# Kernel optimization log

Measured on AMD Instinct MI355X. Metric: run time of the kernel, lower is better.

## Reference

```python
import jax, jax.numpy as jnp
import numpy as np

B, S, D, H, W, FFN = 2, 4096, 1024, 16, 256, 4096
HD = D // H


def layer_norm(x, g, b):
    mu = x.mean(-1, keepdims=True)
    var = ((x - mu) ** 2).mean(-1, keepdims=True)
    return (x - mu) * jax.lax.rsqrt(var + 1e-5) * g + b


def setup_inputs() -> dict:
    key = jax.random.key(0)
    ks = jax.random.split(key, 16)
    s = 1.0 / np.sqrt(D)
    inp = {
        "x": jax.random.normal(ks[0], (B, S, D), jnp.float32),
        "Wq": jax.random.normal(ks[1], (D, D), jnp.float32) * s,
        "bq": jnp.zeros((D,), jnp.float32),
        "Wk": jax.random.normal(ks[2], (D, D), jnp.float32) * s,
        "bk": jnp.zeros((D,), jnp.float32),
        "Wv": jax.random.normal(ks[3], (D, D), jnp.float32) * s,
        "bv": jnp.zeros((D,), jnp.float32),
        "Wo": jax.random.normal(ks[4], (D, D), jnp.float32) * s,
        "bo": jnp.zeros((D,), jnp.float32),
        "g1": jnp.ones((D,), jnp.float32),
        "b1": jnp.zeros((D,), jnp.float32),
        "W1": jax.random.normal(ks[5], (D, FFN), jnp.float32) * s,
        "c1": jnp.zeros((FFN,), jnp.float32),
        "W2": jax.random.normal(ks[6], (FFN, D), jnp.float32) * (1.0 / np.sqrt(FFN)),
        "c2": jnp.zeros((D,), jnp.float32),
        "g2": jnp.ones((D,), jnp.float32),
        "b2": jnp.zeros((D,), jnp.float32),
    }
    return inp


def sliding_window_attn(x, Wq, bq, Wk, bk, Wv, bv, Wo, bo):
    b, s, d = x.shape
    nb = s // W
    # project and chunk into blocks of size W: (B, nb, W, H, HD)
    q = (x @ Wq + bq).reshape(b, nb, W, H, HD)
    k = (x @ Wk + bk).reshape(b, nb, W, H, HD)
    v = (x @ Wv + bv).reshape(b, nb, W, H, HD)
    pad = [(0, 0), (1, 1), (0, 0), (0, 0), (0, 0)]
    kp, vp = jnp.pad(k, pad), jnp.pad(v, pad)
    # each block attends to [prev, self, next] blocks -> (B, nb, 3W, H, HD)
    kc = jnp.concatenate([kp[:, :-2], kp[:, 1:-1], kp[:, 2:]], axis=2)
    vc = jnp.concatenate([vp[:, :-2], vp[:, 1:-1], vp[:, 2:]], axis=2)
    scale = jnp.asarray(1.0 / np.sqrt(HD), x.dtype)
    scores = jnp.einsum("bnqhd,bnkhd->bhnqk", q, kc) * scale
    i = jnp.arange(W)[:, None]
    j = jnp.arange(3 * W)[None, :]
    band = jnp.abs(i + W - j) <= W  # (W, 3W): |q_pos - k_pos| <= W
    kidx = jnp.arange(nb)[:, None] * W - W + jnp.arange(3 * W)[None, :]
    valid = (kidx >= 0) & (kidx < s)  # (nb, 3W): drop padded halo blocks
    mask = band[None, :, :] & valid[:, None, :]  # (nb, W, 3W)
    scores = jnp.where(mask[None, None], scores, jnp.asarray(-1e9, x.dtype))
    attn = jax.nn.softmax(scores, axis=-1)
    out = jnp.einsum("bhnqk,bnkhd->bnqhd", attn, vc).reshape(b, s, d)
    return out @ Wo + bo


def reference(x, Wq, bq, Wk, bk, Wv, bv, Wo, bo, g1, b1, W1, c1, W2, c2, g2, b2):
    a = sliding_window_attn(x, Wq, bq, Wk, bk, Wv, bv, Wo, bo)
    h = layer_norm(a + x, g1, b1)  # dropout = identity (eval mode)
    f = jax.nn.gelu(h @ W1 + c1) @ W2 + c2
    return layer_norm(f + h, g2, b2)
```

## Files before the change

### kernel.cpp

```cpp
#include <hip/hip_runtime.h>
#include <hip/hip_bf16.h>

#define BB 2
#define SS 4096
#define DD 1024
#define HH 16
#define WW 256
#define FF 4096
#define HDIM 64
#define NBLK (SS / WW)
#define MROWS (BB * SS)

typedef short bfrag8 __attribute__((ext_vector_type(8)));
typedef float floatx4 __attribute__((ext_vector_type(4)));

__device__ __forceinline__ float bf2f(ushort u) {
    union { uint i; float f; } c; c.i = ((uint)u) << 16; return c.f;
}
__device__ __forceinline__ ushort f2bf(float f) {
    union { float f; uint i; } c; c.f = f;
    uint r = (c.i + 0x7FFFu + ((c.i >> 16) & 1u)) >> 16;
    return (ushort)r;
}
__device__ __forceinline__ float gelu_tanh(float x) {
    float x3 = x * x * x;
    return 0.5f * x * (1.f + tanhf(0.7978845608028654f * (x + 0.044715f * x3)));
}

__device__ __forceinline__ void gload_lds16(const ushort* g, ushort* l) {
    __builtin_amdgcn_global_load_lds(
        (const __attribute__((address_space(1))) void*)g,
        (__attribute__((address_space(3))) void*)l, 16, 0, 0);
}

__global__ __launch_bounds__(256) void cvt_f32_bf16(
    const float* __restrict__ in, ushort* __restrict__ out)
{
    size_t i = ((size_t)blockIdx.x * 256 + threadIdx.x) * 4;
    float4 v = *(const float4*)(in + i);
    union { ushort u[4]; uint2 d; } t;
    t.u[0] = f2bf(v.x); t.u[1] = f2bf(v.y);
    t.u[2] = f2bf(v.z); t.u[3] = f2bf(v.w);
    *(uint2*)(out + i) = t.d;
}

__global__ __launch_bounds__(256) void cvt_transpose(
    const float* __restrict__ in, ushort* __restrict__ out, int K, int N)
{
    __shared__ ushort sT[32][33];
    const int n0 = blockIdx.x * 32, k0 = blockIdx.y * 32;
    const int r  = threadIdx.x >> 3;
    const int c4 = (threadIdx.x & 7) * 4;

    float4 v = *(const float4*)(in + (size_t)(k0 + r) * N + n0 + c4);
    sT[c4 + 0][r] = f2bf(v.x);
    sT[c4 + 1][r] = f2bf(v.y);
    sT[c4 + 2][r] = f2bf(v.z);
    sT[c4 + 3][r] = f2bf(v.w);
    __syncthreads();
    union { ushort u[4]; uint2 d; } t;
#pragma unroll
    for (int e = 0; e < 4; ++e) t.u[e] = sT[r][c4 + e];
    *(uint2*)(out + (size_t)(n0 + r) * K + k0 + c4) = t.d;
}

__global__ __launch_bounds__(256) void gemm_bt(
    const ushort* __restrict__ A, const ushort* __restrict__ Bt,
    const float* __restrict__ bias, ushort* __restrict__ C,
    int M, int N, int K, int act)
{
    __shared__ ushort sA[128 * 32];
    __shared__ ushort sB[128 * 32];

    const int tid  = threadIdx.x;
    const int m0   = blockIdx.y * 128;
    const int n0   = blockIdx.x * 128;
    const int wave = tid >> 6;
    const int lane = tid & 63;
    const int wm   = (wave >> 1) * 64;
    const int wn   = (wave & 1) * 64;
    const int lrow = lane & 15;
    const int quad = lane >> 4;

    floatx4 acc[4][4];
#pragma unroll
    for (int i = 0; i < 4; ++i)
#pragma unroll
        for (int j = 0; j < 4; ++j)
            acc[i][j] = (floatx4){0.f, 0.f, 0.f, 0.f};

    for (int k0 = 0; k0 < K; k0 += 32) {
#pragma unroll
        for (int it = 0; it < 2; ++it) {
            int c = it * 256 + tid;
            gload_lds16(A  + (size_t)(m0 + (c >> 2)) * K + k0 + (c & 3) * 8, &sA[c * 8]);
            gload_lds16(Bt + (size_t)(n0 + (c >> 2)) * K + k0 + (c & 3) * 8, &sB[c * 8]);
        }
        __syncthreads();

        bfrag8 af[4], bfv[4];
#pragma unroll
        for (int mt = 0; mt < 4; ++mt)
            af[mt] = *(const bfrag8*)&sA[(wm + mt * 16 + lrow) * 32 + quad * 8];
#pragma unroll
        for (int nt = 0; nt < 4; ++nt)
            bfv[nt] = *(const bfrag8*)&sB[(wn + nt * 16 + lrow) * 32 + quad * 8];
#pragma unroll
        for (int mt = 0; mt < 4; ++mt)
#pragma unroll
            for (int nt = 0; nt < 4; ++nt)
                acc[mt][nt] = __builtin_amdgcn_mfma_f32_16x16x32_bf16(
                    af[mt], bfv[nt], acc[mt][nt], 0, 0, 0);
        __syncthreads();
    }

#pragma unroll
    for (int nt = 0; nt < 4; ++nt) {
        int col = n0 + wn + nt * 16 + lrow;
        float bb = bias[col];
#pragma unroll
        for (int mt = 0; mt < 4; ++mt) {
#pragma unroll
            for (int r = 0; r < 4; ++r) {
                int row = m0 + wm + mt * 16 + (quad << 2) + r;
                float v = acc[mt][nt][r] + bb;
                if (act) v = gelu_tanh(v);
                C[(size_t)row * N + col] = f2bf(v);
            }
        }
    }
}

__global__ __launch_bounds__(256) void gemm_qkv(
    const ushort* __restrict__ A, const ushort* __restrict__ Bt,
    const float* __restrict__ bq, const float* __restrict__ bk,
    const float* __restrict__ bv,
    ushort* __restrict__ qb, ushort* __restrict__ kb, ushort* __restrict__ vT)
{
    __shared__ ushort sA[128 * 32];
    __shared__ ushort sB[128 * 32];
    const int K = DD, N = 3 * DD;

    const int tid  = threadIdx.x;
    const int m0   = blockIdx.y * 128;
    const int n0   = blockIdx.x * 128;
    const int wave = tid >> 6;
    const int lane = tid & 63;
    const int wm   = (wave >> 1) * 64;
    const int wn   = (wave & 1) * 64;
    const int lrow = lane & 15;
    const int quad = lane >> 4;

    floatx4 acc[4][4];
#pragma unroll
    for (int i = 0; i < 4; ++i)
#pragma unroll
        for (int j = 0; j < 4; ++j)
            acc[i][j] = (floatx4){0.f, 0.f, 0.f, 0.f};

    for (int k0 = 0; k0 < K; k0 += 32) {
#pragma unroll
        for (int it = 0; it < 2; ++it) {
            int c = it * 256 + tid;
            gload_lds16(A  + (size_t)(m0 + (c >> 2)) * K + k0 + (c & 3) * 8, &sA[c * 8]);
            gload_lds16(Bt + (size_t)(n0 + (c >> 2)) * K + k0 + (c & 3) * 8, &sB[c * 8]);
        }
        __syncthreads();

        bfrag8 af[4], bfv[4];
#pragma unroll
        for (int mt = 0; mt < 4; ++mt)
            af[mt] = *(const bfrag8*)&sA[(wm + mt * 16 + lrow) * 32 + quad * 8];
#pragma unroll
        for (int nt = 0; nt < 4; ++nt)
            bfv[nt] = *(const bfrag8*)&sB[(wn + nt * 16 + lrow) * 32 + quad * 8];
#pragma unroll
        for (int mt = 0; mt < 4; ++mt)
#pragma unroll
            for (int nt = 0; nt < 4; ++nt)
                acc[mt][nt] = __builtin_amdgcn_mfma_f32_16x16x32_bf16(
                    af[mt], bfv[nt], acc[mt][nt], 0, 0, 0);
        __syncthreads();
    }

    const int colbase = n0 + wn;
    const int sel = colbase >> 10;
    if (sel < 2) {
        ushort* C = (sel == 0) ? qb : kb;
        const float* bias = (sel == 0) ? bq : bk;
#pragma unroll
        for (int nt = 0; nt < 4; ++nt) {
            int cc = (colbase + nt * 16 + lrow) & 1023;
            float bb = bias[cc];
#pragma unroll
            for (int mt = 0; mt < 4; ++mt)
#pragma unroll
                for (int r = 0; r < 4; ++r) {
                    int row = m0 + wm + mt * 16 + (quad << 2) + r;
                    C[(size_t)row * DD + cc] = f2bf(acc[mt][nt][r] + bb);
                }
        }
    } else {
#pragma unroll
        for (int nt = 0; nt < 4; ++nt) {
            int cc = (colbase + nt * 16 + lrow) & 1023;
            int h = cc >> 6, dh = cc & 63;
            float bb = bv[cc];
#pragma unroll
            for (int mt = 0; mt < 4; ++mt) {
                int row0 = m0 + wm + mt * 16 + (quad << 2);
                int b = row0 >> 12, s = row0 & 4095;
                union { ushort u[4]; uint2 d; } t;
#pragma unroll
                for (int r = 0; r < 4; ++r) t.u[r] = f2bf(acc[mt][nt][r] + bb);
                *(uint2*)(vT + (size_t)(((b * HH + h) * HDIM + dh)) * SS + s) = t.d;
            }
        }
    }
}

__global__ __launch_bounds__(64, 2) void attn_flash(
    const ushort* __restrict__ q, const ushort* __restrict__ k,
    const ushort* __restrict__ vT, ushort* __restrict__ out)
{
    __shared__ ushort sP[64 * 72];

    const int qt = blockIdx.x, h = blockIdx.y, b = blockIdx.z;
    const int lane = threadIdx.x;
    const int c16  = lane & 15;
    const int quad = lane >> 4;
    const float CC = 0.18033688011112042f;

    bfrag8 qf[4][2];
    {
        const size_t qbase = ((size_t)b * SS + qt * 64) * DD + h * HDIM;
#pragma unroll
        for (int nt = 0; nt < 4; ++nt)
#pragma unroll
            for (int ks = 0; ks < 2; ++ks)
                qf[nt][ks] = *(const bfrag8*)(q + qbase +
                    (size_t)(nt * 16 + c16) * DD + ks * 32 + quad * 8);
    }

    floatx4 oacc[4][4];
#pragma unroll
    for (int i = 0; i < 4; ++i)
#pragma unroll
        for (int j = 0; j < 4; ++j)
            oacc[i][j] = (floatx4){0.f, 0.f, 0.f, 0.f};
    float mrow[4], lsum[4];
#pragma unroll
    for (int i = 0; i < 4; ++i) { mrow[i] = -1e30f; lsum[i] = 0.f; }

    const int st0 = (qt - 4 > 0) ? qt - 4 : 0;
    const int st1 = (qt + 4 < 63) ? qt + 4 : 63;
    const size_t kb_b  = (size_t)b * SS * DD + h * HDIM;
    const size_t vT_b  = (size_t)((b * HH + h) * HDIM) * SS;

    for (int st = st0; st <= st1; ++st) {
        const int dlt = st - qt;

        floatx4 sacc[4][4];
#pragma unroll
        for (int i = 0; i < 4; ++i)
#pragma unroll
            for (int j = 0; j < 4; ++j)
                sacc[i][j] = (floatx4){0.f, 0.f, 0.f, 0.f};
#pragma unroll
        for (int ks = 0; ks < 2; ++ks) {
            bfrag8 kf[4];
#pragma unroll
            for (int mt = 0; mt < 4; ++mt)
                kf[mt] = *(const bfrag8*)(k + kb_b +
                    (size_t)(st * 64 + mt * 16 + c16) * DD + ks * 32 + quad * 8);
#pragma unroll
            for (int mt = 0; mt < 4; ++mt)
#pragma unroll
                for (int nt = 0; nt < 4; ++nt)
                    sacc[mt][nt] = __builtin_amdgcn_mfma_f32_16x16x32_bf16(
                        kf[mt], qf[nt][ks], sacc[mt][nt], 0, 0, 0);
        }

        if (dlt == 4 || dlt == -4) {
#pragma unroll
            for (int mt = 0; mt < 4; ++mt)
#pragma unroll
                for (int nt = 0; nt < 4; ++nt)
#pragma unroll
                    for (int r = 0; r < 4; ++r) {
                        int kl = mt * 16 + quad * 4 + r;
                        int ql = nt * 16 + c16;
                        bool ok = (dlt < 0) ? (kl >= ql) : (kl <= ql);
                        if (!ok) sacc[mt][nt][r] = -1e30f;
                    }
        }

        float pm[4];
#pragma unroll
        for (int nt = 0; nt < 4; ++nt) {
            float a0 = fmaxf(fmaxf(sacc[0][nt][0], sacc[0][nt][1]),
                             fmaxf(sacc[0][nt][2], sacc[0][nt][3]));
            float a1 = fmaxf(fmaxf(sacc[1][nt][0], sacc[1][nt][1]),
                             fmaxf(sacc[1][nt][2], sacc[1][nt][3]));
            float a2 = fmaxf(fmaxf(sacc[2][nt][0], sacc[2][nt][1]),
                             fmaxf(sacc[2][nt][2], sacc[2][nt][3]));
            float a3 = fmaxf(fmaxf(sacc[3][nt][0], sacc[3][nt][1]),
                             fmaxf(sacc[3][nt][2], sacc[3][nt][3]));
            pm[nt] = fmaxf(fmaxf(a0, a1), fmaxf(a2, a3));
            pm[nt] = fmaxf(pm[nt], __shfl_xor(pm[nt], 16, 64));
            pm[nt] = fmaxf(pm[nt], __shfl_xor(pm[nt], 32, 64));
        }
        float al[4];
#pragma unroll
        for (int nt = 0; nt < 4; ++nt) {
            float mn = fmaxf(mrow[nt], pm[nt]);
            al[nt] = exp2f((mrow[nt] - mn) * CC);
            mrow[nt] = mn;
        }
        float ps[4] = {0.f, 0.f, 0.f, 0.f};
#pragma unroll
        for (int mt = 0; mt < 4; ++mt)
#pragma unroll
            for (int nt = 0; nt < 4; ++nt)
#pragma unroll
                for (int r = 0; r < 4; ++r) {
                    float p = exp2f((sacc[mt][nt][r] - mrow[nt]) * CC);
                    sacc[mt][nt][r] = p;
                    ps[nt] += p;
                }
#pragma unroll
        for (int nt = 0; nt < 4; ++nt) {
            ps[nt] += __shfl_xor(ps[nt], 16, 64);
            ps[nt] += __shfl_xor(ps[nt], 32, 64);
            lsum[nt] = lsum[nt] * al[nt] + ps[nt];
        }

#pragma unroll
        for (int mt = 0; mt < 4; ++mt)
#pragma unroll
            for (int nt = 0; nt < 4; ++nt) {
                int row = nt * 16 + c16;
                int g   = (2 * mt + (quad >> 1)) ^ (row & 3);
                union { ushort u[4]; uint2 d; } t;
#pragma unroll
                for (int r = 0; r < 4; ++r) t.u[r] = f2bf(sacc[mt][nt][r]);
                *(uint2*)&sP[row * 72 + g * 8 + (quad & 1) * 4] = t.d;
            }

#pragma unroll
        for (int dt = 0; dt < 4; ++dt)
#pragma unroll
            for (int nq = 0; nq < 4; ++nq)
#pragma unroll
                for (int r = 0; r < 4; ++r)
                    oacc[dt][nq][r] *= al[nq];

#pragma unroll
        for (int ks = 0; ks < 2; ++ks) {
            bfrag8 vf[4], pf[4];
#pragma unroll
            for (int dt = 0; dt < 4; ++dt)
                vf[dt] = *(const bfrag8*)(vT + vT_b +
                    (size_t)(dt * 16 + c16) * SS + st * 64 + ks * 32 + quad * 8);
#pragma unroll
            for (int nq = 0; nq < 4; ++nq) {
                int row = nq * 16 + c16;
                int g   = (4 * ks + quad) ^ (row & 3);
                pf[nq] = *(const bfrag8*)&sP[row * 72 + g * 8];
            }
#pragma unroll
            for (int dt = 0; dt < 4; ++dt)
#pragma unroll
                for (int nq = 0; nq < 4; ++nq)
                    oacc[dt][nq] = __builtin_amdgcn_mfma_f32_16x16x32_bf16(
                        vf[dt], pf[nq], oacc[dt][nq], 0, 0, 0);
        }
    }

#pragma unroll
    for (int nq = 0; nq < 4; ++nq) {
        float inv = 1.f / lsum[nq];
        size_t rbase = ((size_t)b * SS + qt * 64 + nq * 16 + c16) * DD + h * HDIM;
#pragma unroll
        for (int dt = 0; dt < 4; ++dt) {
            union { ushort u[4]; uint2 d; } t;
#pragma unroll
            for (int r = 0; r < 4; ++r) t.u[r] = f2bf(oacc[dt][nq][r] * inv);
            *(uint2*)(out + rbase + dt * 16 + quad * 4) = t.d;
        }
    }
}

__device__ __forceinline__ float ldv(const float* p)  { return *p; }
__device__ __forceinline__ float ldv(const ushort* p) { return bf2f(*p); }
__device__ __forceinline__ void  stv(float* p, float v)  { *p = v; }
__device__ __forceinline__ void  stv(ushort* p, float v) { *p = f2bf(v); }

template <typename RT, typename OT>
__global__ __launch_bounds__(256) void add_ln(
    const ushort* __restrict__ a, const RT* __restrict__ res,
    const float* __restrict__ g, const float* __restrict__ bb,
    OT* __restrict__ out)
{
    const int row = blockIdx.x;
    const int tid = threadIdx.x;
    const size_t base = (size_t)row * DD + tid * 4;

    float x[4];
    float s1 = 0.f, s2 = 0.f;
#pragma unroll
    for (int e = 0; e < 4; ++e) {
        x[e] = bf2f(a[base + e]) + ldv(res + base + e);
        s1 += x[e];
        s2 += x[e] * x[e];
    }
#pragma unroll
    for (int off = 32; off > 0; off >>= 1) {
        s1 += __shfl_down(s1, off, 64);
        s2 += __shfl_down(s2, off, 64);
    }
    __shared__ float r1[4], r2[4];
    const int wave = tid >> 6, lane = tid & 63;
    if (lane == 0) { r1[wave] = s1; r2[wave] = s2; }
    __syncthreads();
    float t1 = r1[0] + r1[1] + r1[2] + r1[3];
    float t2 = r2[0] + r2[1] + r2[2] + r2[3];
    float mu  = t1 * (1.f / DD);
    float var = t2 * (1.f / DD) - mu * mu;
    float rs  = rsqrtf(var + 1e-5f);

#pragma unroll
    for (int e = 0; e < 4; ++e) {
        int col = tid * 4 + e;
        float y = (x[e] - mu) * rs * g[col] + bb[col];
        stv(out + base + e, y);
    }
}

extern "C" void kernel_launch(void* const* d_in, const int* in_sizes, int n_in,
                              void* d_out, int out_size, void* d_ws, size_t ws_size,
                              hipStream_t stream)
{
    (void)in_sizes; (void)n_in; (void)out_size; (void)ws_size;

    const float* x  = (const float*)d_in[0];
    const float* Wq = (const float*)d_in[1];
    const float* bq = (const float*)d_in[2];
    const float* Wk = (const float*)d_in[3];
    const float* bk = (const float*)d_in[4];
    const float* Wv = (const float*)d_in[5];
    const float* bv = (const float*)d_in[6];
    const float* Wo = (const float*)d_in[7];
    const float* bo = (const float*)d_in[8];
    const float* g1 = (const float*)d_in[9];
    const float* b1 = (const float*)d_in[10];
    const float* W1 = (const float*)d_in[11];
    const float* c1 = (const float*)d_in[12];
    const float* W2 = (const float*)d_in[13];
    const float* c2 = (const float*)d_in[14];
    const float* g2 = (const float*)d_in[15];
    const float* b2 = (const float*)d_in[16];
    float* outp = (float*)d_out;

    char* ws = (char*)d_ws;
    const size_t MB = 1024 * 1024;
    ushort* WqkvT = (ushort*)(ws);
    ushort* WoT = (ushort*)(ws + 6  * MB);
    ushort* W1t = (ushort*)(ws + 8  * MB);
    ushort* W2t = (ushort*)(ws + 16 * MB);
    ushort* xb  = (ushort*)(ws + 24 * MB);
    ushort* qb  = (ushort*)(ws + 40 * MB);
    ushort* kb  = (ushort*)(ws + 56 * MB);
    ushort* vT  = (ushort*)(ws + 72 * MB);
    ushort* att = (ushort*)(ws + 88 * MB);
    ushort* aproj = qb;
    ushort* hbuf  = att;
    ushort* m1  = (ushort*)(ws + 24 * MB);
    ushort* fbuf = (ushort*)(ws + 104 * MB);

    dim3 blk(256, 1, 1);
    dim3 gD(DD / 128, MROWS / 128, 1);
    dim3 gQKV(3 * DD / 128, MROWS / 128, 1);
    dim3 gF(FF / 128, MROWS / 128, 1);
    dim3 ga(SS / 64, HH, BB);
    dim3 gl(MROWS, 1, 1);

    hipLaunchKernelGGL(cvt_transpose, dim3(32, 32),  blk, 0, stream, Wq, WqkvT, DD, DD);
    hipLaunchKernelGGL(cvt_transpose, dim3(32, 32),  blk, 0, stream, Wk, WqkvT + 1024 * 1024, DD, DD);
    hipLaunchKernelGGL(cvt_transpose, dim3(32, 32),  blk, 0, stream, Wv, WqkvT + 2 * 1024 * 1024, DD, DD);
    hipLaunchKernelGGL(cvt_transpose, dim3(32, 32),  blk, 0, stream, Wo, WoT, DD, DD);
    hipLaunchKernelGGL(cvt_transpose, dim3(128, 32), blk, 0, stream, W1, W1t, DD, FF);
    hipLaunchKernelGGL(cvt_transpose, dim3(32, 128), blk, 0, stream, W2, W2t, FF, DD);
    hipLaunchKernelGGL(cvt_f32_bf16, dim3(8192), blk, 0, stream, x, xb);

    hipLaunchKernelGGL(gemm_qkv, gQKV, blk, 0, stream, xb, WqkvT, bq, bk, bv, qb, kb, vT);

    hipLaunchKernelGGL(attn_flash, ga, dim3(64, 1, 1), 0, stream, qb, kb, vT, att);

    hipLaunchKernelGGL(gemm_bt, gD, blk, 0, stream, att, WoT, bo, aproj, MROWS, DD, DD, 0);
    hipLaunchKernelGGL((add_ln<float, ushort>), gl, blk, 0, stream, aproj, x, g1, b1, hbuf);

    hipLaunchKernelGGL(gemm_bt, gF, blk, 0, stream, hbuf, W1t, c1, m1, MROWS, FF, DD, 1);
    hipLaunchKernelGGL(gemm_bt, gD, blk, 0, stream, m1, W2t, c2, fbuf, MROWS, DD, FF, 0);
    hipLaunchKernelGGL((add_ln<ushort, float>), gl, blk, 0, stream, fbuf, hbuf, g2, b2, outp);
}
```

Baseline: 584.8 us.

## Merge weight transposes, vectorize GEMM epilogue stores, use exp-based GELU

Measured after the change: 573.8 us. About the same (-1.9%).

```diff
diff --git a/kernel.cpp b/kernel.cpp
--- a/kernel.cpp
+++ b/kernel.cpp
@@ -22,9 +22,9 @@
     uint r = (c.i + 0x7FFFu + ((c.i >> 16) & 1u)) >> 16;
     return (ushort)r;
 }
-__device__ __forceinline__ float gelu_tanh(float x) {
-    float x3 = x * x * x;
-    return 0.5f * x * (1.f + tanhf(0.7978845608028654f * (x + 0.044715f * x3)));
+__device__ __forceinline__ float gelu_fast(float x) {
+    float z2 = 1.5957691216057308f * x * (1.f + 0.044715f * x * x);
+    return x / (1.f + __expf(-z2));
 }
 
 __device__ __forceinline__ void gload_lds16(const ushort* g, ushort* l) {
@@ -44,11 +44,30 @@
     *(uint2*)(out + i) = t.d;
 }
 
-__global__ __launch_bounds__(256) void cvt_transpose(
-    const float* __restrict__ in, ushort* __restrict__ out, int K, int N)
+__global__ __launch_bounds__(256) void cvt_transpose_all(
+    const float* __restrict__ Wq, const float* __restrict__ Wk,
+    const float* __restrict__ Wv, const float* __restrict__ Wo,
+    const float* __restrict__ W1, const float* __restrict__ W2,
+    ushort* __restrict__ WqkvT, ushort* __restrict__ WoT,
+    ushort* __restrict__ W1t, ushort* __restrict__ W2t)
 {
     __shared__ ushort sT[32][33];
-    const int n0 = blockIdx.x * 32, k0 = blockIdx.y * 32;
+    const int z = blockIdx.z;
+    const float* in; ushort* out; int K, N, n0, k0;
+    if (z < 4) {
+        if (blockIdx.x >= 32) return;
+        in  = (z == 0) ? Wq : (z == 1) ? Wk : (z == 2) ? Wv : Wo;
+        out = (z < 3) ? WqkvT + (size_t)z * 1024 * 1024 : WoT;
+        K = 1024; N = 1024;
+        n0 = blockIdx.x * 32; k0 = blockIdx.y * 32;
+    } else if (z == 4) {
+        in = W1; out = W1t; K = 1024; N = 4096;
+        n0 = blockIdx.x * 32; k0 = blockIdx.y * 32;
+    } else {
+        in = W2; out = W2t; K = 4096; N = 1024;
+        n0 = blockIdx.y * 32; k0 = blockIdx.x * 32;
+    }
+
     const int r  = threadIdx.x >> 3;
     const int c4 = (threadIdx.x & 7) * 4;
 
@@ -110,23 +129,26 @@
 #pragma unroll
             for (int nt = 0; nt < 4; ++nt)
                 acc[mt][nt] = __builtin_amdgcn_mfma_f32_16x16x32_bf16(
-                    af[mt], bfv[nt], acc[mt][nt], 0, 0, 0);
+                    bfv[nt], af[mt], acc[mt][nt], 0, 0, 0);
         __syncthreads();
     }
 
 #pragma unroll
     for (int nt = 0; nt < 4; ++nt) {
-        int col = n0 + wn + nt * 16 + lrow;
-        float bb = bias[col];
+        int nb = n0 + wn + nt * 16 + quad * 4;
+        union { float4 v; float f[4]; } b4;
+        b4.v = *(const float4*)(bias + nb);
 #pragma unroll
         for (int mt = 0; mt < 4; ++mt) {
+            int row = m0 + wm + mt * 16 + lrow;
+            union { ushort u[4]; uint2 d; } t;
 #pragma unroll
             for (int r = 0; r < 4; ++r) {
-                int row = m0 + wm + mt * 16 + (quad << 2) + r;
-                float v = acc[mt][nt][r] + bb;
-                if (act) v = gelu_tanh(v);
-                C[(size_t)row * N + col] = f2bf(v);
-            }
+                float v = acc[mt][nt][r] + b4.f[r];
+                if (act) v = gelu_fast(v);
+                t.u[r] = f2bf(v);
+            }
+            *(uint2*)(C + (size_t)row * N + nb) = t.d;
         }
     }
 }
@@ -139,7 +161,7 @@
 {
     __shared__ ushort sA[128 * 32];
     __shared__ ushort sB[128 * 32];
-    const int K = DD, N = 3 * DD;
+    const int K = DD;
 
     const int tid  = threadIdx.x;
     const int m0   = blockIdx.y * 128;
@@ -150,6 +172,7 @@
     const int wn   = (wave & 1) * 64;
     const int lrow = lane & 15;
     const int quad = lane >> 4;
+    const int sel  = n0 >> 10;
 
     floatx4 acc[4][4];
 #pragma unroll
@@ -158,49 +181,72 @@
         for (int j = 0; j < 4; ++j)
             acc[i][j] = (floatx4){0.f, 0.f, 0.f, 0.f};
 
-    for (int k0 = 0; k0 < K; k0 += 32) {
-#pragma unroll
-        for (int it = 0; it < 2; ++it) {
-            int c = it * 256 + tid;
-            gload_lds16(A  + (size_t)(m0 + (c >> 2)) * K + k0 + (c & 3) * 8, &sA[c * 8]);
-            gload_lds16(Bt + (size_t)(n0 + (c >> 2)) * K + k0 + (c & 3) * 8, &sB[c * 8]);
-        }
-        __syncthreads();
-
-        bfrag8 af[4], bfv[4];
-#pragma unroll
-        for (int mt = 0; mt < 4; ++mt)
-            af[mt] = *(const bfrag8*)&sA[(wm + mt * 16 + lrow) * 32 + quad * 8];
-#pragma unroll
-        for (int nt = 0; nt < 4; ++nt)
-            bfv[nt] = *(const bfrag8*)&sB[(wn + nt * 16 + lrow) * 32 + quad * 8];
-#pragma unroll
-        for (int mt = 0; mt < 4; ++mt)
+    if (sel < 2) {
+        for (int k0 = 0; k0 < K; k0 += 32) {
+#pragma unroll
+            for (int it = 0; it < 2; ++it) {
+                int c = it * 256 + tid;
+                gload_lds16(A  + (size_t)(m0 + (c >> 2)) * K + k0 + (c & 3) * 8, &sA[c * 8]);
+                gload_lds16(Bt + (size_t)(n0 + (c >> 2)) * K + k0 + (c & 3) * 8, &sB[c * 8]);
+            }
+            __syncthreads();
+            bfrag8 af[4], bfv[4];
+#pragma unroll
+            for (int mt = 0; mt < 4; ++mt)
+                af[mt] = *(const bfrag8*)&sA[(wm + mt * 16 + lrow) * 32 + quad * 8];
 #pragma unroll
             for (int nt = 0; nt < 4; ++nt)
-                acc[mt][nt] = __builtin_amdgcn_mfma_f32_16x16x32_bf16(
-                    af[mt], bfv[nt], acc[mt][nt], 0, 0, 0);
-        __syncthreads();
-    }
-
-    const int colbase = n0 + wn;
-    const int sel = colbase >> 10;
-    if (sel < 2) {
+                bfv[nt] = *(const bfrag8*)&sB[(wn + nt * 16 + lrow) * 32 + quad * 8];
+#pragma unroll
+            for (int mt = 0; mt < 4; ++mt)
+#pragma unroll
+                for (int nt = 0; nt < 4; ++nt)
+                    acc[mt][nt] = __builtin_amdgcn_mfma_f32_16x16x32_bf16(
+                        bfv[nt], af[mt], acc[mt][nt], 0, 0, 0);
+            __syncthreads();
+        }
         ushort* C = (sel == 0) ? qb : kb;
         const float* bias = (sel == 0) ? bq : bk;
+        const int colbase = n0 + wn;
 #pragma unroll
         for (int nt = 0; nt < 4; ++nt) {
-            int cc = (colbase + nt * 16 + lrow) & 1023;
-            float bb = bias[cc];
-#pragma unroll
-            for (int mt = 0; mt < 4; ++mt)
-#pragma unroll
-                for (int r = 0; r < 4; ++r) {
-                    int row = m0 + wm + mt * 16 + (quad << 2) + r;
-                    C[(size_t)row * DD + cc] = f2bf(acc[mt][nt][r] + bb);
-                }
+            int nb = (colbase + nt * 16 + quad * 4) & 1023;
+            union { float4 v; float f[4]; } b4;
+            b4.v = *(const float4*)(bias + nb);
+#pragma unroll
+            for (int mt = 0; mt < 4; ++mt) {
+                int row = m0 + wm + mt * 16 + lrow;
+                union { ushort u[4]; uint2 d; } t;
+#pragma unroll
+                for (int r = 0; r < 4; ++r) t.u[r] = f2bf(acc[mt][nt][r] + b4.f[r]);
+                *(uint2*)(C + (size_t)row * DD + nb) = t.d;
+            }
         }
     } else {
+        for (int k0 = 0; k0 < K; k0 += 32) {
+#pragma unroll
+            for (int it = 0; it < 2; ++it) {
+                int c = it * 256 + tid;
+                gload_lds16(A  + (size_t)(m0 + (c >> 2)) * K + k0 + (c & 3) * 8, &sA[c * 8]);
+                gload_lds16(Bt + (size_t)(n0 + (c >> 2)) * K + k0 + (c & 3) * 8, &sB[c * 8]);
+            }
+            __syncthreads();
+            bfrag8 af[4], bfv[4];
+#pragma unroll
+            for (int mt = 0; mt < 4; ++mt)
+                af[mt] = *(const bfrag8*)&sA[(wm + mt * 16 + lrow) * 32 + quad * 8];
+#pragma unroll
+            for (int nt = 0; nt < 4; ++nt)
+                bfv[nt] = *(const bfrag8*)&sB[(wn + nt * 16 + lrow) * 32 + quad * 8];
+#pragma unroll
+            for (int mt = 0; mt < 4; ++mt)
+#pragma unroll
+                for (int nt = 0; nt < 4; ++nt)
+                    acc[mt][nt] = __builtin_amdgcn_mfma_f32_16x16x32_bf16(
+                        af[mt], bfv[nt], acc[mt][nt], 0, 0, 0);
+            __syncthreads();
+        }
+        const int colbase = n0 + wn;
 #pragma unroll
         for (int nt = 0; nt < 4; ++nt) {
             int cc = (colbase + nt * 16 + lrow) & 1023;
@@ -485,12 +531,8 @@
     dim3 ga(SS / 64, HH, BB);
     dim3 gl(MROWS, 1, 1);
 
-    hipLaunchKernelGGL(cvt_transpose, dim3(32, 32),  blk, 0, stream, Wq, WqkvT, DD, DD);
-    hipLaunchKernelGGL(cvt_transpose, dim3(32, 32),  blk, 0, stream, Wk, WqkvT + 1024 * 1024, DD, DD);
-    hipLaunchKernelGGL(cvt_transpose, dim3(32, 32),  blk, 0, stream, Wv, WqkvT + 2 * 1024 * 1024, DD, DD);
-    hipLaunchKernelGGL(cvt_transpose, dim3(32, 32),  blk, 0, stream, Wo, WoT, DD, DD);
-    hipLaunchKernelGGL(cvt_transpose, dim3(128, 32), blk, 0, stream, W1, W1t, DD, FF);
-    hipLaunchKernelGGL(cvt_transpose, dim3(32, 128), blk, 0, stream, W2, W2t, FF, DD);
+    hipLaunchKernelGGL(cvt_transpose_all, dim3(128, 32, 6), blk, 0, stream,
+                       Wq, Wk, Wv, Wo, W1, W2, WqkvT, WoT, W1t, W2t);
     hipLaunchKernelGGL(cvt_f32_bf16, dim3(8192), blk, 0, stream, x, xb);
 
     hipLaunchKernelGGL(gemm_qkv, gQKV, blk, 0, stream, xb, WqkvT, bq, bk, bv, qb, kb, vT);
```
